# Kernel optimization log

Measured on AMD Instinct MI355X. Metric: run time of the kernel, lower is better.

The kernel has to match this reference:

```python
import jax, jax.numpy as jnp
import numpy as np

N_TOKENS = 16384
INPUT_DIM = 4096
N_EXPERTS = 64
TOP_K = 8
EPS = 1e-12  # torch F.normalize eps
SCALE = 5.0


def l2_normalize(v):
    # matches torch.nn.functional.normalize(p=2, dim=-1, eps=1e-12)
    norm = jnp.sqrt(jnp.sum(v * v, axis=-1, keepdims=True))
    return v / jnp.maximum(norm, EPS)


def setup_inputs() -> dict:
    key = jax.random.key(0)
    kx, ks = jax.random.split(key)
    x = jax.random.normal(kx, (N_TOKENS, INPUT_DIM), dtype=jnp.float32)
    # signatures are L2-normalized in the module (_normalize_signatures)
    sig = jax.random.normal(ks, (N_EXPERTS, INPUT_DIM), dtype=jnp.float32)
    phase_signatures = l2_normalize(sig)
    return {"x": x, "phase_signatures": phase_signatures}


def reference(x, phase_signatures):
    x_norm = l2_normalize(x)                                   # [N, D]
    resonance = jnp.einsum('nd,ed->ne', x_norm, phase_signatures)  # [N, E]
    resonance = resonance * SCALE
    k = min(TOP_K, resonance.shape[-1])
    top_k_resonance, top_k_indices = jax.lax.top_k(resonance, k)   # [N, k]
    weights = jax.nn.softplus(top_k_resonance)                 # [N, k]
    return (weights, top_k_indices, resonance)
```

## Files before the change

### kernel.cpp

```cpp
#include <hip/hip_runtime.h>
#include <cmath>


#define N_TOKENS 16384
#define DIM      4096
#define NE       64
#define TOPK     8
#define SCALE    5.0f
#define EPS      1e-12f
#define NS       32

typedef short  frag   __attribute__((ext_vector_type(8)));
typedef float  f32x16 __attribute__((ext_vector_type(16)));
typedef int    i32x4  __attribute__((ext_vector_type(4)));
typedef short  short4v __attribute__((ext_vector_type(4)));

__device__ __forceinline__ void split3(float v, unsigned& h1, unsigned& h2, unsigned& h3) {
    unsigned u  = __builtin_bit_cast(unsigned, v);
    unsigned r1 = (u + 0x7FFFu + ((u >> 16) & 1u)) & 0xFFFF0000u;
    float    d1 = v - __builtin_bit_cast(float, r1);
    unsigned w  = __builtin_bit_cast(unsigned, d1);
    unsigned r2 = (w + 0x7FFFu + ((w >> 16) & 1u)) & 0xFFFF0000u;
    float    d2 = d1 - __builtin_bit_cast(float, r2);
    unsigned z  = __builtin_bit_cast(unsigned, d2);
    unsigned r3 = (z + 0x7FFFu + ((z >> 16) & 1u)) & 0xFFFF0000u;
    h1 = r1 >> 16; h2 = r2 >> 16; h3 = r3 >> 16;
}

__launch_bounds__(256)
__global__ void convert_sig(const float* __restrict__ sig,
                            short* __restrict__ h1,
                            short* __restrict__ h2,
                            short* __restrict__ h3) {
    const int tid = blockIdx.x * 256 + threadIdx.x;
    const int e   = tid >> 10;
    const int kq  = (tid & 1023) << 2;
    const float4 v = *(const float4*)(sig + (size_t)e * DIM + kq);
    const float vs[4] = {v.x, v.y, v.z, v.w};
    const int tile = e >> 5, e31 = e & 31;
    const int kb = kq >> 4, hf = (kq >> 3) & 1, off = kq & 7;
    const int lane = (hf << 5) | e31;
    const int base = ((tile * 256 + kb) * 64 + lane) * 8 + off;
    short4v o1, o2, o3;
#pragma unroll
    for (int p = 0; p < 4; ++p) {
        unsigned a, b, c;
        split3(vs[p], a, b, c);
        o1[p] = (short)a; o2[p] = (short)b; o3[p] = (short)c;
    }
    *(short4v*)(h1 + base) = o1;
    *(short4v*)(h2 + base) = o2;
    *(short4v*)(h3 + base) = o3;
}

__launch_bounds__(512, 4)
__global__ void gemm_fused(const float* __restrict__ x,
                           const short* __restrict__ sh1,
                           const short* __restrict__ sh2,
                           const short* __restrict__ sh3,
                           float* __restrict__ outR) {
    __shared__ float red[4][64][34];
    __shared__ float sqred[8][32];
    __shared__ float scl[32];

    const int t    = threadIdx.x;
    const int lane = t & 63;
    const int w    = t >> 6;
    const int l31  = lane & 31;
    const int half = lane >> 5;

    const int tb = blockIdx.x * 32;
    const int k0 = w * (DIM / 8);

    const float* ap = x + (size_t)(tb + l31) * DIM + k0 + 8 * half;
    const int bbase = ((w * NS) * 64 + lane) * 8;
    const short* b1p = sh1 + bbase;
    const short* b2p = sh2 + bbase;
    const short* b3p = sh3 + bbase;
    const int TILE1 = 256 * 64 * 8;

    f32x16 c0 = {};
    f32x16 c1 = {};
    float sq = 0.f;

    float4 cur0 = *(const float4*)(ap);
    float4 cur1 = *(const float4*)(ap + 4);
    float4 nxt0 = *(const float4*)(ap + 16);
    float4 nxt1 = *(const float4*)(ap + 20);

#pragma unroll 2
    for (int st = 0; st < NS; ++st) {
        const frag b1a = *(const frag*)(b1p);
        const frag b1b = *(const frag*)(b1p + TILE1);
        const frag b2a = *(const frag*)(b2p);
        const frag b2b = *(const frag*)(b2p + TILE1);
        const frag b3a = *(const frag*)(b3p);
        const frag b3b = *(const frag*)(b3p + TILE1);

        float4 f0 = cur0, f1 = cur1;
        if (st + 2 < NS) {
            f0 = *(const float4*)(ap + 32);
            f1 = *(const float4*)(ap + 36);
        }

        const float vals[8] = {cur0.x, cur0.y, cur0.z, cur0.w,
                               cur1.x, cur1.y, cur1.z, cur1.w};
        i32x4 a1i, a2i, a3i;
#pragma unroll
        for (int p = 0; p < 4; ++p) {
            const float v0 = vals[2 * p], v1 = vals[2 * p + 1];
            sq = fmaf(v0, v0, sq);
            sq = fmaf(v1, v1, sq);
            unsigned h10, h20, h30, h11, h21, h31;
            split3(v0, h10, h20, h30);
            split3(v1, h11, h21, h31);
            a1i[p] = (int)(h10 | (h11 << 16));
            a2i[p] = (int)(h20 | (h21 << 16));
            a3i[p] = (int)(h30 | (h31 << 16));
        }
        const frag A1 = __builtin_bit_cast(frag, a1i);
        const frag A2 = __builtin_bit_cast(frag, a2i);
        const frag A3 = __builtin_bit_cast(frag, a3i);

        c0 = __builtin_amdgcn_mfma_f32_32x32x16_bf16(A1, b1a, c0, 0, 0, 0);
        c1 = __builtin_amdgcn_mfma_f32_32x32x16_bf16(A1, b1b, c1, 0, 0, 0);
        c0 = __builtin_amdgcn_mfma_f32_32x32x16_bf16(A1, b2a, c0, 0, 0, 0);
        c1 = __builtin_amdgcn_mfma_f32_32x32x16_bf16(A1, b2b, c1, 0, 0, 0);
        c0 = __builtin_amdgcn_mfma_f32_32x32x16_bf16(A2, b1a, c0, 0, 0, 0);
        c1 = __builtin_amdgcn_mfma_f32_32x32x16_bf16(A2, b1b, c1, 0, 0, 0);
        c0 = __builtin_amdgcn_mfma_f32_32x32x16_bf16(A1, b3a, c0, 0, 0, 0);
        c1 = __builtin_amdgcn_mfma_f32_32x32x16_bf16(A1, b3b, c1, 0, 0, 0);
        c0 = __builtin_amdgcn_mfma_f32_32x32x16_bf16(A3, b1a, c0, 0, 0, 0);
        c1 = __builtin_amdgcn_mfma_f32_32x32x16_bf16(A3, b1b, c1, 0, 0, 0);
        c0 = __builtin_amdgcn_mfma_f32_32x32x16_bf16(A2, b2a, c0, 0, 0, 0);
        c1 = __builtin_amdgcn_mfma_f32_32x32x16_bf16(A2, b2b, c1, 0, 0, 0);

        cur0 = nxt0; cur1 = nxt1; nxt0 = f0; nxt1 = f1;
        ap += 16; b1p += 512; b2p += 512; b3p += 512;
    }

    sq += __shfl_xor(sq, 32);
    if (lane < 32) sqred[w][l31] = sq;

    if (w >= 4) {
#pragma unroll
        for (int r = 0; r < 16; ++r) {
            red[w - 4][lane][r]      = c0[r];
            red[w - 4][lane][16 + r] = c1[r];
        }
    }
    __syncthreads();

    if (t < 32) {
        float q = 0.f;
#pragma unroll
        for (int ww = 0; ww < 8; ++ww) q += sqred[ww][t];
        scl[t] = SCALE / fmaxf(sqrtf(q), EPS);
    }

    if (w < 4) {
#pragma unroll
        for (int r = 0; r < 16; ++r) {
            const float s0 = c0[r] + red[w][lane][r];
            const float s1 = c1[r] + red[w][lane][16 + r];
            red[w][lane][r]      = s0;
            red[w][lane][16 + r] = s1;
        }
    }
    __syncthreads();

    const int wm = w & 3, tile = w >> 2;
    const int et = l31 + 32 * tile;
#pragma unroll
    for (int j = 0; j < 4; ++j) {
        const int R = 4 * w + j;
        const float a = red[0][lane][R] + red[1][lane][R] +
                        red[2][lane][R] + red[3][lane][R];
        const int token = j + 8 * wm + 4 * half;
        outR[(size_t)(tb + token) * NE + et] = a * scl[token];
    }
}

__launch_bounds__(256)
__global__ void topk_wave(const float* __restrict__ outR,
                          float* __restrict__ outW,
                          float* __restrict__ outI) {
    const int t    = threadIdx.x;
    const int lane = t & 63;
    const int w    = t >> 6;
    const int tok  = blockIdx.x * 4 + w;

    const float v = outR[(size_t)tok * NE + lane];
    const unsigned u = __builtin_bit_cast(unsigned, v);
    const unsigned s = u ^ ((unsigned)(((int)u) >> 31) | 0x80000000u);
    unsigned long long cur = ((unsigned long long)s << 32) | (unsigned)(63 - lane);

    float bw = 0.f;
    int   bi = 0;
#pragma unroll
    for (int m = 0; m < TOPK; ++m) {
        unsigned long long r = cur;
#pragma unroll
        for (int d = 32; d >= 1; d >>= 1) {
            const unsigned long long o = __shfl_xor(r, d);
            r = (o > r) ? o : r;
        }
        const int we = 63 - (int)(r & 63ull);
        const float bv = __shfl(v, we);
        if (lane == we) cur = 0ull;
        if (lane == m) { bw = bv; bi = we; }
    }
    if (lane < TOPK) {
        outW[(size_t)tok * TOPK + lane] = log1pf(expf(bw));
        outI[(size_t)tok * TOPK + lane] = (float)bi;
    }
}

extern "C" void kernel_launch(void* const* d_in, const int* in_sizes, int n_in,
                              void* d_out, int out_size, void* d_ws, size_t ws_size,
                              hipStream_t stream) {
    const float* x   = (const float*)d_in[0];
    const float* sig = (const float*)d_in[1];
    float* out  = (float*)d_out;
    float* outW = out;
    float* outI = out + (size_t)N_TOKENS * TOPK;
    float* outR = out + (size_t)N_TOKENS * TOPK * 2;

    const size_t SIGE = (size_t)NE * DIM;
    short* sh1 = (short*)d_ws;
    short* sh2 = sh1 + SIGE;
    short* sh3 = sh2 + SIGE;

    convert_sig<<<256, 256, 0, stream>>>(sig, sh1, sh2, sh3);
    gemm_fused<<<N_TOKENS / 32, 512, 0, stream>>>(x, sh1, sh2, sh3, outR);
    topk_wave<<<N_TOKENS / 4, 256, 0, stream>>>(outR, outW, outI);
}
```

Measured before the change: 404.3 us.

## Fuse top-k selection into GEMM epilogue and widen signature conversion stores

The top-k/softplus kernel is folded into the GEMM epilogue: scaled resonance values are staged in a shared-memory tile, written out with coalesced float4 stores, and each wave then runs the shuffle-based top-8 on four tokens straight from shared memory. This removes a kernel launch and a global re-read of the resonance matrix. The signature conversion kernel now handles 8 elements per thread with 16-byte fragment stores at half the grid size, and the main loop unroll is dropped to 1. The cost is extra shared memory (about 8.7 KB) and a longer serial epilogue per block, which may reduce occupancy.

```diff
diff --git a/kernel.cpp b/kernel.cpp
--- a/kernel.cpp
+++ b/kernel.cpp
@@ -13,7 +13,6 @@
 typedef short  frag   __attribute__((ext_vector_type(8)));
 typedef float  f32x16 __attribute__((ext_vector_type(16)));
 typedef int    i32x4  __attribute__((ext_vector_type(4)));
-typedef short  short4v __attribute__((ext_vector_type(4)));
 
 __device__ __forceinline__ void split3(float v, unsigned& h1, unsigned& h2, unsigned& h3) {
     unsigned u  = __builtin_bit_cast(unsigned, v);
@@ -32,25 +31,26 @@
                             short* __restrict__ h1,
                             short* __restrict__ h2,
                             short* __restrict__ h3) {
-    const int tid = blockIdx.x * 256 + threadIdx.x;
-    const int e   = tid >> 10;
-    const int kq  = (tid & 1023) << 2;
-    const float4 v = *(const float4*)(sig + (size_t)e * DIM + kq);
-    const float vs[4] = {v.x, v.y, v.z, v.w};
-    const int tile = e >> 5, e31 = e & 31;
-    const int kb = kq >> 4, hf = (kq >> 3) & 1, off = kq & 7;
-    const int lane = (hf << 5) | e31;
-    const int base = ((tile * 256 + kb) * 64 + lane) * 8 + off;
-    short4v o1, o2, o3;
-#pragma unroll
-    for (int p = 0; p < 4; ++p) {
+    const int tid  = blockIdx.x * 256 + threadIdx.x;
+    const int lane = tid & 63;
+    const int kb   = (tid >> 6) & 255;
+    const int tile = tid >> 14;
+    const int e31  = lane & 31, hf = lane >> 5;
+    const float* src = sig + (size_t)(tile * 32 + e31) * DIM + kb * 16 + hf * 8;
+    const float4 v0 = *(const float4*)(src);
+    const float4 v1 = *(const float4*)(src + 4);
+    const float vs[8] = {v0.x, v0.y, v0.z, v0.w, v1.x, v1.y, v1.z, v1.w};
+    frag o1, o2, o3;
+#pragma unroll
+    for (int p = 0; p < 8; ++p) {
         unsigned a, b, c;
         split3(vs[p], a, b, c);
         o1[p] = (short)a; o2[p] = (short)b; o3[p] = (short)c;
     }
-    *(short4v*)(h1 + base) = o1;
-    *(short4v*)(h2 + base) = o2;
-    *(short4v*)(h3 + base) = o3;
+    const int base = ((tile * 256 + kb) * 64 + lane) * 8;
+    *(frag*)(h1 + base) = o1;
+    *(frag*)(h2 + base) = o2;
+    *(frag*)(h3 + base) = o3;
 }
 
 __launch_bounds__(512, 4)
@@ -58,8 +58,11 @@
                            const short* __restrict__ sh1,
                            const short* __restrict__ sh2,
                            const short* __restrict__ sh3,
-                           float* __restrict__ outR) {
+                           float* __restrict__ outR,
+                           float* __restrict__ outW,
+                           float* __restrict__ outI) {
     __shared__ float red[4][64][34];
+    __shared__ float res[32][68];
     __shared__ float sqred[8][32];
     __shared__ float scl[32];
 
@@ -88,7 +91,7 @@
     float4 nxt0 = *(const float4*)(ap + 16);
     float4 nxt1 = *(const float4*)(ap + 20);
 
-#pragma unroll 2
+#pragma unroll 1
     for (int st = 0; st < NS; ++st) {
         const frag b1a = *(const frag*)(b1p);
         const frag b1b = *(const frag*)(b1p + TILE1);
@@ -161,10 +164,8 @@
     if (w < 4) {
 #pragma unroll
         for (int r = 0; r < 16; ++r) {
-            const float s0 = c0[r] + red[w][lane][r];
-            const float s1 = c1[r] + red[w][lane][16 + r];
-            red[w][lane][r]      = s0;
-            red[w][lane][16 + r] = s1;
+            red[w][lane][r]      = c0[r] + red[w][lane][r];
+            red[w][lane][16 + r] = c1[r] + red[w][lane][16 + r];
         }
     }
     __syncthreads();
@@ -177,42 +178,44 @@
         const float a = red[0][lane][R] + red[1][lane][R] +
                         red[2][lane][R] + red[3][lane][R];
         const int token = j + 8 * wm + 4 * half;
-        outR[(size_t)(tb + token) * NE + et] = a * scl[token];
-    }
-}
-
-__launch_bounds__(256)
-__global__ void topk_wave(const float* __restrict__ outR,
-                          float* __restrict__ outW,
-                          float* __restrict__ outI) {
-    const int t    = threadIdx.x;
-    const int lane = t & 63;
-    const int w    = t >> 6;
-    const int tok  = blockIdx.x * 4 + w;
-
-    const float v = outR[(size_t)tok * NE + lane];
-    const unsigned u = __builtin_bit_cast(unsigned, v);
-    const unsigned s = u ^ ((unsigned)(((int)u) >> 31) | 0x80000000u);
-    unsigned long long cur = ((unsigned long long)s << 32) | (unsigned)(63 - lane);
-
-    float bw = 0.f;
-    int   bi = 0;
-#pragma unroll
-    for (int m = 0; m < TOPK; ++m) {
-        unsigned long long r = cur;
-#pragma unroll
-        for (int d = 32; d >= 1; d >>= 1) {
-            const unsigned long long o = __shfl_xor(r, d);
-            r = (o > r) ? o : r;
-        }
-        const int we = 63 - (int)(r & 63ull);
-        const float bv = __shfl(v, we);
-        if (lane == we) cur = 0ull;
-        if (lane == m) { bw = bv; bi = we; }
-    }
-    if (lane < TOPK) {
-        outW[(size_t)tok * TOPK + lane] = log1pf(expf(bw));
-        outI[(size_t)tok * TOPK + lane] = (float)bi;
+        res[token][et] = a * scl[token];
+    }
+    __syncthreads();
+
+    {
+        const int token = t >> 4, q4 = (t & 15) * 4;
+        *(float4*)(outR + (size_t)(tb + token) * NE + q4) =
+            *(const float4*)(&res[token][q4]);
+    }
+
+#pragma unroll 1
+    for (int tt = 0; tt < 4; ++tt) {
+        const int token = 4 * w + tt;
+        const float v = res[token][lane];
+        const unsigned u = __builtin_bit_cast(unsigned, v);
+        const unsigned s = u ^ ((unsigned)(((int)u) >> 31) | 0x80000000u);
+        unsigned long long cur = ((unsigned long long)s << 32) | (unsigned)(63 - lane);
+
+        float bw = 0.f;
+        int   bi = 0;
+#pragma unroll
+        for (int m = 0; m < TOPK; ++m) {
+            unsigned long long r = cur;
+#pragma unroll
+            for (int d = 32; d >= 1; d >>= 1) {
+                const unsigned long long o = __shfl_xor(r, d);
+                r = (o > r) ? o : r;
+            }
+            const int we = 63 - (int)(r & 63ull);
+            const float bv = __shfl(v, we);
+            if (lane == we) cur = 0ull;
+            if (lane == m) { bw = bv; bi = we; }
+        }
+        if (lane < TOPK) {
+            const size_t ob = (size_t)(tb + token) * TOPK + lane;
+            outW[ob] = log1pf(expf(bw));
+            outI[ob] = (float)bi;
+        }
     }
 }
 
@@ -231,7 +234,6 @@
     short* sh2 = sh1 + SIGE;
     short* sh3 = sh2 + SIGE;
 
-    convert_sig<<<256, 256, 0, stream>>>(sig, sh1, sh2, sh3);
-    gemm_fused<<<N_TOKENS / 32, 512, 0, stream>>>(x, sh1, sh2, sh3, outR);
-    topk_wave<<<N_TOKENS / 4, 256, 0, stream>>>(outR, outW, outI);
-}
+    convert_sig<<<128, 256, 0, stream>>>(sig, sh1, sh2, sh3);
+    gemm_fused<<<N_TOKENS / 32, 512, 0, stream>>>(x, sh1, sh2, sh3, outR, outW, outI);
+}
```

Result: no change. 396.6 us (-1.9%).
